# Optimization experiments

Hardware: AMD Instinct MI355X
Metric: run time of the kernel (lower is better)

Reference implementation:

```python
import jax, jax.numpy as jnp
import numpy as np

N_NODES = 100000
N_EDGES = 1600000
IN_CH = 128
HEADS = 8
OUT_CH = 8  # per head; concat -> 64


def setup_inputs() -> dict:
    key = jax.random.key(0)
    ks = jax.random.split(key, 6)
    x = jax.random.normal(ks[0], (N_NODES, IN_CH), dtype=jnp.float32)
    W = jax.random.normal(ks[1], (IN_CH, HEADS * OUT_CH), dtype=jnp.float32) * (IN_CH ** -0.5)
    att_src = jax.random.normal(ks[2], (1, HEADS, OUT_CH), dtype=jnp.float32) * (OUT_CH ** -0.5)
    att_dst = jax.random.normal(ks[3], (1, HEADS, OUT_CH), dtype=jnp.float32) * (OUT_CH ** -0.5)
    bias = jnp.zeros((HEADS * OUT_CH,), dtype=jnp.float32)
    edge_index = jax.random.randint(ks[4], (2, N_EDGES), 0, N_NODES, dtype=jnp.int64)
    return {"x": x, "W": W, "att_src": att_src, "att_dst": att_dst,
            "bias": bias, "edge_index": edge_index}


def reference(x, W, att_src, att_dst, bias, edge_index):
    # eval mode: both input dropout (p=0.6) and attention dropout are identity
    N = x.shape[0]
    H, F = att_src.shape[1], att_src.shape[2]
    # linear transform per head: [N, H, F]
    h = (x @ W).reshape(N, H, F)
    # per-node attention logits (PyG GATConv): [N, H]
    a_src = jnp.sum(h * att_src, axis=-1)
    a_dst = jnp.sum(h * att_dst, axis=-1)
    # add self-loops (PyG default add_self_loops=True)
    loop = jnp.arange(N, dtype=edge_index.dtype)
    src = jnp.concatenate([edge_index[0], loop])  # message source j
    dst = jnp.concatenate([edge_index[1], loop])  # message target i
    # edge-wise attention score: [E+N, H]
    e = jax.nn.leaky_relu(a_src[src] + a_dst[dst], 0.2)
    # segment softmax over edges grouped by destination node
    m = jax.ops.segment_max(e, dst, num_segments=N)          # [N, H]
    e = jnp.exp(e - m[dst])
    s = jax.ops.segment_sum(e, dst, num_segments=N)          # [N, H]
    alpha = e / (s[dst] + 1e-16)                             # [E+N, H]
    # scatter-aggregate weighted messages: [N, H, F]
    out = jax.ops.segment_sum(alpha[:, :, None] * h[src], dst, num_segments=N)
    out = out.reshape(N, H * F) + bias
    return jax.nn.elu(out)
```

## Files before the change

### kernel.cpp

```cpp
#include <hip/hip_runtime.h>
#include <cstdint>
#include <cstddef>


#define PAD 48

typedef __attribute__((ext_vector_type(8))) short short8v;
typedef __attribute__((ext_vector_type(4))) float f32x4;

__device__ __forceinline__ unsigned short f2bf(float f) {
    unsigned u = __float_as_uint(f);
    unsigned r = u + 0x7FFFu + ((u >> 16) & 1u);
    return (unsigned short)(r >> 16);
}
__device__ __forceinline__ float bf2f(unsigned short u) {
    return __uint_as_float(((unsigned)u) << 16);
}

__global__ __launch_bounds__(256) void gat_linear_scatter(
    const float* __restrict__ x, const float* __restrict__ W,
    const float* __restrict__ att_src, const float* __restrict__ att_dst,
    unsigned short* __restrict__ h_bf, float* __restrict__ a_src,
    float* __restrict__ a_dst, const int* __restrict__ e_src,
    const int* __restrict__ e_dst, int* __restrict__ deg,
    int* __restrict__ esrc, int N, int E, int nChunksE, int nLin)
{
    __shared__ unsigned short Wt[64][136];
    const int bid = (int)blockIdx.x;
    const int tid = threadIdx.x;
    const int g   = bid >> 6;
    const int rem = bid & 63;

    if (rem < 56) {
        const int chunk = g * 7 + (rem >> 3);
        if (chunk >= nChunksE) return;
        const int range = rem & 7;
        const int lo = (int)(((long long)N * range) >> 3);
        const int hi = (int)(((long long)N * (range + 1)) >> 3);

        const int b = chunk * 1024 + tid * 4;
        if (b + 3 < E) {
            int4 sv = *reinterpret_cast<const int4*>(e_src + b);
            int4 dv = *reinterpret_cast<const int4*>(e_dst + b);
            if (dv.x >= lo && dv.x < hi) esrc[dv.x * PAD + atomicAdd(&deg[dv.x], 1)] = sv.x;
            if (dv.y >= lo && dv.y < hi) esrc[dv.y * PAD + atomicAdd(&deg[dv.y], 1)] = sv.y;
            if (dv.z >= lo && dv.z < hi) esrc[dv.z * PAD + atomicAdd(&deg[dv.z], 1)] = sv.z;
            if (dv.w >= lo && dv.w < hi) esrc[dv.w * PAD + atomicAdd(&deg[dv.w], 1)] = sv.w;
        } else {
            for (int k = b; k < E; ++k) {
                int d = e_dst[k];
                if (d >= lo && d < hi) esrc[d * PAD + atomicAdd(&deg[d], 1)] = e_src[k];
            }
        }
        return;
    }

    const int lin = g * 8 + rem - 56;
    if (lin >= nLin) return;
    const int lane = tid & 63;
    const int wi   = tid >> 6;

    for (int i = tid; i < 8192; i += 256) {
        const int k = i >> 6, col = i & 63;
        Wt[col][k] = f2bf(W[i]);
    }
    __syncthreads();

    const int r0   = lin * 64 + wi * 16;
    const int lrow = lane & 15;
    const int kgrp = (lane >> 4) * 8;
    const int row  = r0 + lrow;
    const int rowc = row < N ? row : N - 1;

    short8v bf[4][4];
    #pragma unroll
    for (int t = 0; t < 4; ++t)
        #pragma unroll
        for (int c = 0; c < 4; ++c)
            bf[t][c] = *reinterpret_cast<const short8v*>(&Wt[lrow + 16 * c][t * 32 + kgrp]);

    const float* xr = x + (size_t)rowc * 128 + kgrp;
    float4 xa[4][2];
    #pragma unroll
    for (int t = 0; t < 4; ++t) {
        xa[t][0] = *reinterpret_cast<const float4*>(xr + t * 32);
        xa[t][1] = *reinterpret_cast<const float4*>(xr + t * 32 + 4);
    }

    f32x4 acc[4] = {f32x4{0,0,0,0}, f32x4{0,0,0,0}, f32x4{0,0,0,0}, f32x4{0,0,0,0}};
    #pragma unroll
    for (int t = 0; t < 4; ++t) {
        short8v af;
        af[0] = (short)f2bf(xa[t][0].x); af[1] = (short)f2bf(xa[t][0].y);
        af[2] = (short)f2bf(xa[t][0].z); af[3] = (short)f2bf(xa[t][0].w);
        af[4] = (short)f2bf(xa[t][1].x); af[5] = (short)f2bf(xa[t][1].y);
        af[6] = (short)f2bf(xa[t][1].z); af[7] = (short)f2bf(xa[t][1].w);
        #pragma unroll
        for (int c = 0; c < 4; ++c)
            acc[c] = __builtin_amdgcn_mfma_f32_16x16x32_bf16(af, bf[t][c], acc[c], 0, 0, 0);
    }

    const int gg = lane >> 4;
    float attS[4], attD[4];
    #pragma unroll
    for (int c = 0; c < 4; ++c) {
        attS[c] = att_src[lrow + 16 * c];
        attD[c] = att_dst[lrow + 16 * c];
    }

    #pragma unroll
    for (int reg = 0; reg < 4; ++reg) {
        const int r = r0 + gg * 4 + reg;
        if (r < N) {
            #pragma unroll
            for (int c = 0; c < 4; ++c) {
                const float v = acc[c][reg];
                h_bf[(size_t)r * 64 + lrow + 16 * c] = f2bf(v);
                float vs = v * attS[c];
                float vd = v * attD[c];
                vs += __shfl_xor(vs, 1, 64); vd += __shfl_xor(vd, 1, 64);
                vs += __shfl_xor(vs, 2, 64); vd += __shfl_xor(vd, 2, 64);
                vs += __shfl_xor(vs, 4, 64); vd += __shfl_xor(vd, 4, 64);
                if ((lane & 7) == 0) {
                    const int head = ((lane & 8) >> 3) + 2 * c;
                    a_src[r * 8 + head] = vs;
                    a_dst[r * 8 + head] = vd;
                }
            }
        }
    }
}

__global__ __launch_bounds__(256) void gat_gather(
    const int* __restrict__ deg, const int* __restrict__ esrc,
    const unsigned short* __restrict__ h_bf, const float* __restrict__ a_src,
    const float* __restrict__ a_dst, const float* __restrict__ bias,
    float* __restrict__ out, int N)
{
    const int node = blockIdx.x * 4 + (threadIdx.x >> 6);
    if (node >= N) return;
    const int lane = threadIdx.x & 63;
    const int head = lane >> 3;
    const int sub  = lane & 7;
    const int gbase = lane & 56;

    const float ad = a_dst[node * 8 + head];
    float e0 = a_src[node * 8 + head] + ad;
    e0 = e0 > 0.f ? e0 : 0.2f * e0;
    float w0 = __expf(e0);
    float acc = w0 * bf2f(h_bf[(uint32_t)node * 64u + (uint32_t)lane]);
    float s = w0;

    const int cnt = deg[node];
    const int beg = node * PAD;
    for (int k = 0; k < cnt; k += 8) {
        const int ke = k + sub;
        const int kc = ke < cnt ? ke : cnt - 1;
        const int sm = esrc[beg + kc];
        float a = a_src[(uint32_t)sm * 8u + (uint32_t)head] + ad;
        a = a > 0.f ? a : 0.2f * a;
        const float wm = (ke < cnt) ? __expf(a) : 0.f;

        uint32_t hoff[8];
        #pragma unroll
        for (int u = 0; u < 8; ++u) {
            const int sb = __shfl(sm, gbase | u, 64);
            hoff[u] = (uint32_t)sb * 64u + (uint32_t)lane;
        }
        float hb[8];
        #pragma unroll
        for (int u = 0; u < 8; ++u) hb[u] = bf2f(h_bf[hoff[u]]);

        #pragma unroll
        for (int u = 0; u < 8; ++u) {
            const float w = __shfl(wm, gbase | u, 64);
            acc += w * hb[u];
            s += w;
        }
    }

    float v = acc / (s + 1e-16f) + bias[lane];
    out[(uint32_t)node * 64u + (uint32_t)lane] = v > 0.f ? v : expm1f(v);
}

extern "C" void kernel_launch(void* const* d_in, const int* in_sizes, int n_in,
                              void* d_out, int out_size, void* d_ws, size_t ws_size,
                              hipStream_t stream)
{
    const float* x       = (const float*)d_in[0];
    const float* W       = (const float*)d_in[1];
    const float* att_src = (const float*)d_in[2];
    const float* att_dst = (const float*)d_in[3];
    const float* bias    = (const float*)d_in[4];
    const int*   ei      = (const int*)d_in[5];

    const int N = in_sizes[0] / 128;
    const int E = in_sizes[5] / 2;

    float* out = (float*)d_out;

    unsigned short* h_bf = (unsigned short*)d_ws;
    float* a_src    = (float*)(h_bf + (size_t)N * 64);
    float* a_dst    = a_src + (size_t)N * 8;
    int*   deg      = (int*)(a_dst + (size_t)N * 8);
    int*   esrc     = deg + N;

    const int* e_src = ei;
    const int* e_dst = ei + E;

    hipMemsetAsync(deg, 0, (size_t)N * sizeof(int), stream);

    const int nChunksE = (E + 1023) / 1024;
    const int nLin     = (N + 63) / 64;
    const int gc       = (nChunksE + 6) / 7;
    const int gl       = (nLin + 7) / 8;
    const int nSuper   = gc > gl ? gc : gl;
    gat_linear_scatter<<<nSuper * 64, 256, 0, stream>>>(
        x, W, att_src, att_dst, h_bf, a_src, a_dst,
        e_src, e_dst, deg, esrc, N, E, nChunksE, nLin);

    gat_gather<<<(N + 3) / 4, 256, 0, stream>>>(deg, esrc, h_bf, a_src, a_dst, bias, out, N);
}
```

Before: 152.7 us.

## Split fused linear/scatter kernel into separate linear and scatter launches

The combined kernel, which interleaved MFMA linear-transform blocks with edge-bucketing scatter blocks in one grid, is split into two kernels launched one after the other. This drops the block-index dispatch and the interleaved schedule, and gives each kernel its own grid sizing and register/LDS footprint. In exchange the two phases no longer overlap on the GPU, and there is an extra launch.

```diff
diff --git a/kernel.cpp b/kernel.cpp
--- a/kernel.cpp
+++ b/kernel.cpp
@@ -17,46 +17,14 @@
     return __uint_as_float(((unsigned)u) << 16);
 }
 
-__global__ __launch_bounds__(256) void gat_linear_scatter(
+__global__ __launch_bounds__(256) void gat_linear(
     const float* __restrict__ x, const float* __restrict__ W,
     const float* __restrict__ att_src, const float* __restrict__ att_dst,
     unsigned short* __restrict__ h_bf, float* __restrict__ a_src,
-    float* __restrict__ a_dst, const int* __restrict__ e_src,
-    const int* __restrict__ e_dst, int* __restrict__ deg,
-    int* __restrict__ esrc, int N, int E, int nChunksE, int nLin)
+    float* __restrict__ a_dst, int N)
 {
     __shared__ unsigned short Wt[64][136];
-    const int bid = (int)blockIdx.x;
-    const int tid = threadIdx.x;
-    const int g   = bid >> 6;
-    const int rem = bid & 63;
-
-    if (rem < 56) {
-        const int chunk = g * 7 + (rem >> 3);
-        if (chunk >= nChunksE) return;
-        const int range = rem & 7;
-        const int lo = (int)(((long long)N * range) >> 3);
-        const int hi = (int)(((long long)N * (range + 1)) >> 3);
-
-        const int b = chunk * 1024 + tid * 4;
-        if (b + 3 < E) {
-            int4 sv = *reinterpret_cast<const int4*>(e_src + b);
-            int4 dv = *reinterpret_cast<const int4*>(e_dst + b);
-            if (dv.x >= lo && dv.x < hi) esrc[dv.x * PAD + atomicAdd(&deg[dv.x], 1)] = sv.x;
-            if (dv.y >= lo && dv.y < hi) esrc[dv.y * PAD + atomicAdd(&deg[dv.y], 1)] = sv.y;
-            if (dv.z >= lo && dv.z < hi) esrc[dv.z * PAD + atomicAdd(&deg[dv.z], 1)] = sv.z;
-            if (dv.w >= lo && dv.w < hi) esrc[dv.w * PAD + atomicAdd(&deg[dv.w], 1)] = sv.w;
-        } else {
-            for (int k = b; k < E; ++k) {
-                int d = e_dst[k];
-                if (d >= lo && d < hi) esrc[d * PAD + atomicAdd(&deg[d], 1)] = e_src[k];
-            }
-        }
-        return;
-    }
-
-    const int lin = g * 8 + rem - 56;
-    if (lin >= nLin) return;
+    const int tid  = threadIdx.x;
     const int lane = tid & 63;
     const int wi   = tid >> 6;
 
@@ -66,7 +34,7 @@
     }
     __syncthreads();
 
-    const int r0   = lin * 64 + wi * 16;
+    const int r0   = blockIdx.x * 64 + wi * 16;
     const int lrow = lane & 15;
     const int kgrp = (lane >> 4) * 8;
     const int row  = r0 + lrow;
@@ -131,6 +99,31 @@
     }
 }
 
+__global__ __launch_bounds__(256) void gat_scatter(
+    const int* __restrict__ e_src, const int* __restrict__ e_dst,
+    int* __restrict__ deg, int* __restrict__ esrc, int E, int N)
+{
+    const int range = blockIdx.x & 7;
+    const int chunk = blockIdx.x >> 3;
+    const int lo = (int)(((long long)N * range) >> 3);
+    const int hi = (int)(((long long)N * (range + 1)) >> 3);
+
+    const int b = chunk * 1024 + threadIdx.x * 4;
+    if (b + 3 < E) {
+        int4 sv = *reinterpret_cast<const int4*>(e_src + b);
+        int4 dv = *reinterpret_cast<const int4*>(e_dst + b);
+        if (dv.x >= lo && dv.x < hi) esrc[dv.x * PAD + atomicAdd(&deg[dv.x], 1)] = sv.x;
+        if (dv.y >= lo && dv.y < hi) esrc[dv.y * PAD + atomicAdd(&deg[dv.y], 1)] = sv.y;
+        if (dv.z >= lo && dv.z < hi) esrc[dv.z * PAD + atomicAdd(&deg[dv.z], 1)] = sv.z;
+        if (dv.w >= lo && dv.w < hi) esrc[dv.w * PAD + atomicAdd(&deg[dv.w], 1)] = sv.w;
+    } else {
+        for (int k = b; k < E; ++k) {
+            int d = e_dst[k];
+            if (d >= lo && d < hi) esrc[d * PAD + atomicAdd(&deg[d], 1)] = e_src[k];
+        }
+    }
+}
+
 __global__ __launch_bounds__(256) void gat_gather(
     const int* __restrict__ deg, const int* __restrict__ esrc,
     const unsigned short* __restrict__ h_bf, const float* __restrict__ a_src,
@@ -210,14 +203,12 @@
 
     hipMemsetAsync(deg, 0, (size_t)N * sizeof(int), stream);
 
+    const int nLin = (N + 63) / 64;
+    gat_linear<<<nLin, 256, 0, stream>>>(
+        x, W, att_src, att_dst, h_bf, a_src, a_dst, N);
+
     const int nChunksE = (E + 1023) / 1024;
-    const int nLin     = (N + 63) / 64;
-    const int gc       = (nChunksE + 6) / 7;
-    const int gl       = (nLin + 7) / 8;
-    const int nSuper   = gc > gl ? gc : gl;
-    gat_linear_scatter<<<nSuper * 64, 256, 0, stream>>>(
-        x, W, att_src, att_dst, h_bf, a_src, a_dst,
-        e_src, e_dst, deg, esrc, N, E, nChunksE, nLin);
+    gat_scatter<<<nChunksE * 8, 256, 0, stream>>>(e_src, e_dst, deg, esrc, E, N);
 
     gat_gather<<<(N + 3) / 4, 256, 0, stream>>>(deg, esrc, h_bf, a_src, a_dst, bias, out, N);
 }
```

Result: slower. 163.4 us (+7.0%).
